# Optimization experiments

Measured on AMD Instinct MI355X. Metric: run time of the kernel, lower is better.

The kernel has to match this reference:

```python
import jax, jax.numpy as jnp
import numpy as np

N, E, G = 20000, 320000, 128
H, TE, CD = 128, 128, 64
HEADS, DH = 4, 32          # inner = 128 == H
L = 6


def _fwd(p, edge_index, batch):
    """Faithful forward of CrystalDiffusionModel (eval mode: dropout = identity).
    EquivariantGraphConv (imported in the original) is implemented as the standard
    edge-conditioned message-passing conv: m_ij = silu(W[h_src; h_dst; e_ij] + b),
    agg = scatter_add over dst, h' = W_u[h; agg] + b_u."""
    x, ea, t = p['x'], p['edge_attr'], p['t']
    n = x.shape[0]
    h = x @ p['Wn'] + p['bn']                      # [N,H] node embedding
    ef = ea @ p['We'] + p['be']                    # [E,H] edge embedding

    # sinusoidal time embedding -> MLP
    half = TE // 2
    freq = jnp.exp(-jnp.arange(half, dtype=jnp.float32) * (np.log(10000.0) / (half - 1)))
    te = t[:, None] * freq[None, :]
    te = jnp.concatenate([jnp.sin(te), jnp.cos(te)], axis=-1)          # [G,TE]
    te = jax.nn.silu(te @ p['tm_W1'] + p['tm_b1']) @ p['tm_W2'] + p['tm_b2']

    def mlp2(z, W1, b1, W2, b2):
        return jax.nn.silu(z @ W1 + b1) @ W2 + b2

    topo_e = mlp2(p['topo_cond'], p['topo_W1'], p['topo_b1'], p['topo_W2'], p['topo_b2'])
    stab_e = mlp2(p['stab_cond'], p['stab_W1'], p['stab_b1'], p['stab_W2'], p['stab_b2'])
    sust_e = mlp2(p['sust_cond'], p['sust_W1'], p['sust_b1'], p['sust_W2'], p['sust_b2'])
    cond = mlp2(jnp.concatenate([topo_e, stab_e, sust_e], axis=-1),
                p['comb_W1'], p['comb_b1'], p['comb_W2'], p['comb_b2'])  # [G,CD]

    ctx = cond[batch]                               # [N,CD] per-node condition
    # context is a single token per query -> k,v constant across layers
    k = (ctx @ p['Wk']).reshape(n, HEADS, DH)
    v = (ctx @ p['Wv']).reshape(n, HEADS, DH)
    ti = jax.nn.silu(te)[batch]                     # [N,H] time influence (dropout=id)

    src, dst = edge_index[0], edge_index[1]
    scale = DH ** -0.5
    for i in range(L):
        Wm, bm = p['gnn_Wm'][i], p['gnn_bm'][i]
        # split concat-GEMM to avoid materializing [E, 3H]
        m = jax.nn.silu(h[src] @ Wm[:H] + h[dst] @ Wm[H:2 * H] + ef @ Wm[2 * H:] + bm)
        agg = jax.ops.segment_sum(m, dst, num_segments=n)               # [N,H]
        Wu, bu = p['gnn_Wu'][i], p['gnn_bu'][i]
        hu = h @ Wu[:H] + agg @ Wu[H:] + bu
        # LayerNorm
        mu = hu.mean(-1, keepdims=True)
        var = hu.var(-1, keepdims=True)
        hu = (hu - mu) * jax.lax.rsqrt(var + 1e-5) * p['ln_g'][i] + p['ln_b'][i]
        # cross-attention; context length is 1 so softmax over j is exactly 1
        q = (hu @ p['Wq']).reshape(n, HEADS, DH)
        sim = jnp.einsum('nhd,nhd->nh', q, k) * scale                   # [N,heads]
        attn = jax.nn.softmax(sim[..., None], axis=-1)                  # == 1.0
        out = (attn * v).reshape(n, HEADS * DH)
        hu = out @ p['Wo'] + p['bo']
        h = h + hu + ti                              # residual + time influence

    node_pred = jax.nn.silu(h @ p['np_W1'] + p['np_b1']) @ p['np_W2'] + p['np_b2']
    pos_pred = jax.nn.silu(h @ p['pp_W1'] + p['pp_b1']) @ p['pp_W2'] + p['pp_b2']
    return node_pred, pos_pred


def setup_inputs() -> dict:
    key = jax.random.key(0)
    it = iter(jax.random.split(key, 96))

    def nrm(shape, s=0.02):
        return jax.random.normal(next(it), shape, jnp.float32) * s

    z = lambda *s: jnp.zeros(s, jnp.float32)
    inp = {
        'x': jax.random.normal(next(it), (N, 12), jnp.float32),
        'edge_index': jax.random.randint(next(it), (2, E), 0, N),
        'edge_attr': jax.random.normal(next(it), (E, 20), jnp.float32),
        'pos': jax.random.normal(next(it), (N, 3), jnp.float32),
        't': jax.random.uniform(next(it), (G,), jnp.float32) * 1000.0,
        'topo_cond': jax.random.normal(next(it), (G, 7), jnp.float32),
        'stab_cond': jax.random.normal(next(it), (G, 2), jnp.float32),
        'sust_cond': jax.random.normal(next(it), (G, 3), jnp.float32),
        'batch': jnp.sort(jax.random.randint(next(it), (N,), 0, G)),
        'Wn': nrm((12, H)), 'bn': z(H), 'We': nrm((20, H)), 'be': z(H),
        'tm_W1': nrm((TE, 2 * TE)), 'tm_b1': z(2 * TE), 'tm_W2': nrm((2 * TE, TE)), 'tm_b2': z(TE),
        'topo_W1': nrm((7, 32)), 'topo_b1': z(32), 'topo_W2': nrm((32, 32)), 'topo_b2': z(32),
        'stab_W1': nrm((2, 16)), 'stab_b1': z(16), 'stab_W2': nrm((16, 16)), 'stab_b2': z(16),
        'sust_W1': nrm((3, 16)), 'sust_b1': z(16), 'sust_W2': nrm((16, 16)), 'sust_b2': z(16),
        'comb_W1': nrm((64, CD)), 'comb_b1': z(CD), 'comb_W2': nrm((CD, CD)), 'comb_b2': z(CD),
        'Wq': nrm((H, HEADS * DH)), 'Wk': nrm((CD, HEADS * DH)), 'Wv': nrm((CD, HEADS * DH)),
        'Wo': nrm((HEADS * DH, H)), 'bo': z(H),
        'gnn_Wm': nrm((L, 3 * H, H)), 'gnn_bm': z(L, H),
        'gnn_Wu': nrm((L, 2 * H, H)), 'gnn_bu': z(L, H),
        'ln_g': jnp.ones((L, H), jnp.float32), 'ln_b': z(L, H),
        'np_W1': nrm((H, 2 * H)), 'np_b1': z(2 * H), 'np_W2': nrm((2 * H, 12)), 'np_b2': z(12),
        'pp_W1': nrm((H, H)), 'pp_b1': z(H), 'pp_W2': nrm((H, 3)), 'pp_b2': z(3),
    }
    return inp


def reference(x, edge_index, edge_attr, pos, t, topo_cond, stab_cond, sust_cond, batch,
              Wn, bn, We, be, tm_W1, tm_b1, tm_W2, tm_b2,
              topo_W1, topo_b1, topo_W2, topo_b2, stab_W1, stab_b1, stab_W2, stab_b2,
              sust_W1, sust_b1, sust_W2, sust_b2, comb_W1, comb_b1, comb_W2, comb_b2,
              Wq, Wk, Wv, Wo, bo, gnn_Wm, gnn_bm, gnn_Wu, gnn_bu, ln_g, ln_b,
              np_W1, np_b1, np_W2, np_b2, pp_W1, pp_b1, pp_W2, pp_b2):
    loc = dict(locals())
    p = {k: v for k, v in loc.items() if k not in ('edge_index', 'batch', 'pos')}
    return _fwd(p, edge_index, batch)
```

## Files before the change

kernel.cpp:

```cpp
#include <hip/hip_runtime.h>
#include <hip/hip_bf16.h>

#define NN 20000
#define GG 128

typedef __bf16 bf16x8_t __attribute__((ext_vector_type(8)));
typedef float  f32x4_t  __attribute__((ext_vector_type(4)));
typedef __hip_bfloat16 hbf16;

#define PK_NPW1 0
#define PK_PPW1 32768
#define PK_NPW2 49152
#define PK_PPW2 53248
#define PK_WN   55296
#define GADD_OFF 59392

__device__ __forceinline__ float silu_f(float v) {
    return v * __builtin_amdgcn_rcpf(1.0f + __expf(-v));
}

__device__ __forceinline__ void cp_async(hbf16* dst, const hbf16* src,
                                         int nbytes, int w, int lane) {
    const int per_wave = nbytes >> 2;
    const char* g = (const char*)src + w * per_wave + lane * 16;
    char* l = (char*)dst + w * per_wave + lane * 16;
    for (int j = 0; j < per_wave; j += 1024)
        __builtin_amdgcn_global_load_lds(
            (__attribute__((address_space(1))) void*)(g + j),
            (__attribute__((address_space(3))) void*)(l + j),
            16, 0, 0);
}

__global__ __launch_bounds__(512) void prep_kernel(
        const float* __restrict__ t, const float* __restrict__ topo,
        const float* __restrict__ stab, const float* __restrict__ sust,
        const float* __restrict__ tmW1, const float* __restrict__ tmb1,
        const float* __restrict__ tmW2, const float* __restrict__ tmb2,
        const float* __restrict__ topoW1, const float* __restrict__ topob1,
        const float* __restrict__ topoW2, const float* __restrict__ topob2,
        const float* __restrict__ stabW1, const float* __restrict__ stabb1,
        const float* __restrict__ stabW2, const float* __restrict__ stabb2,
        const float* __restrict__ sustW1, const float* __restrict__ sustb1,
        const float* __restrict__ sustW2, const float* __restrict__ sustb2,
        const float* __restrict__ combW1, const float* __restrict__ combb1,
        const float* __restrict__ combW2, const float* __restrict__ combb2,
        const float* __restrict__ Wv, const float* __restrict__ Wo,
        const float* __restrict__ bo,
        const float* __restrict__ npW1, const float* __restrict__ npW2,
        const float* __restrict__ ppW1, const float* __restrict__ ppW2,
        const float* __restrict__ Wn,
        float* __restrict__ gadd, hbf16* __restrict__ wsb) {
    const int tid = threadIdx.x;

    if (blockIdx.x >= GG) {
        const int s = (blockIdx.x - GG) * 512 + tid;
        if (s < 32768) {
            const int p = s;
            const int j = p & 7, l = (p >> 3) & 63, kb = (p >> 9) & 3, ct = p >> 11;
            const int k = kb * 32 + ((l >> 4) << 3) + j;
            const int n = ct * 16 + (l & 15);
            wsb[PK_NPW1 + p] = __float2bfloat16(npW1[k * 256 + n]);
        } else if (s < 49152) {
            const int p = s - 32768;
            const int j = p & 7, l = (p >> 3) & 63, kb = (p >> 9) & 3, ct = p >> 11;
            const int k = kb * 32 + ((l >> 4) << 3) + j;
            const int n = ct * 16 + (l & 15);
            wsb[PK_PPW1 + p] = __float2bfloat16(ppW1[k * 128 + n]);
        } else if (s < 53248) {
            const int p = s - 49152;
            const int j = p & 7, l = (p >> 3) & 63, kb = p >> 9;
            const int k = kb * 32 + ((l >> 4) << 3) + j;
            const int n = l & 15;
            wsb[PK_NPW2 + p] = __float2bfloat16(n < 12 ? npW2[k * 12 + n] : 0.0f);
        } else if (s < 55296) {
            const int p = s - 53248;
            const int j = p & 7, l = (p >> 3) & 63, kb = p >> 9;
            const int k = kb * 32 + ((l >> 4) << 3) + j;
            const int n = l & 15;
            wsb[PK_PPW2 + p] = __float2bfloat16(n < 3 ? ppW2[k * 3 + n] : 0.0f);
        } else if (s < 59392) {
            const int p = s - 55296;
            const int j = p & 7, l = (p >> 3) & 63, ct = p >> 9;
            const int k = ((l >> 4) << 3) + j;
            const int n = ct * 16 + (l & 15);
            wsb[PK_WN + p] = __float2bfloat16(k < 12 ? Wn[k * 128 + n] : 0.0f);
        }
        return;
    }

    __shared__ float s_te[128];
    __shared__ float s_th1[256];
    __shared__ float s_tef[128];
    __shared__ float s_l1[64];
    __shared__ float s_cat[64];
    __shared__ float s_c1[64];
    __shared__ float s_cond[64];
    __shared__ float s_v[128];
    __shared__ float s_red[512];

    const int g = blockIdx.x;

    if (tid < 128) {
        const float tval = t[g];
        const int i = tid & 63;
        const float fr = __expf(-(float)i * 0.14619587892025688f);
        const float arg = tval * fr;
        s_te[tid] = (tid < 64) ? sinf(arg) : cosf(arg);
    } else if (tid < 192) {
        const int c = tid - 128;
        if (c < 32) {
            float acc = topob1[c];
            for (int k = 0; k < 7; ++k)
                acc += topo[g * 7 + k] * topoW1[k * 32 + c];
            s_l1[c] = silu_f(acc);
        } else if (c < 48) {
            const int j = c - 32;
            float acc = stabb1[j];
            for (int k = 0; k < 2; ++k)
                acc += stab[g * 2 + k] * stabW1[k * 16 + j];
            s_l1[c] = silu_f(acc);
        } else {
            const int j = c - 48;
            float acc = sustb1[j];
            for (int k = 0; k < 3; ++k)
                acc += sust[g * 3 + k] * sustW1[k * 16 + j];
            s_l1[c] = silu_f(acc);
        }
    }
    __syncthreads();

    {
        const int col = tid & 255, half = tid >> 8;
        float acc = 0.0f;
#pragma unroll 32
        for (int kk = 0; kk < 64; ++kk) {
            const int k = half * 64 + kk;
            acc += s_te[k] * tmW1[k * 256 + col];
        }
        s_red[half * 256 + col] = acc;
    }
    __syncthreads();
    if (tid < 256)
        s_th1[tid] = silu_f(tmb1[tid] + s_red[tid] + s_red[256 + tid]);
    __syncthreads();

    {
        const int col = tid & 127, qt = tid >> 7;
        float acc = 0.0f;
#pragma unroll 32
        for (int kk = 0; kk < 64; ++kk) {
            const int k = qt * 64 + kk;
            acc += s_th1[k] * tmW2[k * 128 + col];
        }
        s_red[qt * 128 + col] = acc;
    }
    __syncthreads();
    if (tid < 128) {
        s_tef[tid] = tmb2[tid] + s_red[tid] + s_red[128 + tid] +
                     s_red[256 + tid] + s_red[384 + tid];
    } else if (tid < 192) {
        const int c = tid - 128;
        if (c < 32) {
            float acc = topob2[c];
            for (int k = 0; k < 32; ++k)
                acc += s_l1[k] * topoW2[k * 32 + c];
            s_cat[c] = acc;
        } else if (c < 48) {
            const int j = c - 32;
            float acc = stabb2[j];
            for (int k = 0; k < 16; ++k)
                acc += s_l1[32 + k] * stabW2[k * 16 + j];
            s_cat[c] = acc;
        } else {
            const int j = c - 48;
            float acc = sustb2[j];
            for (int k = 0; k < 16; ++k)
                acc += s_l1[48 + k] * sustW2[k * 16 + j];
            s_cat[c] = acc;
        }
    }
    __syncthreads();

    {
        const int col = tid & 63, part = tid >> 6;
        float acc = 0.0f;
#pragma unroll
        for (int kk = 0; kk < 8; ++kk) {
            const int k = part * 8 + kk;
            acc += s_cat[k] * combW1[k * 64 + col];
        }
        s_red[part * 64 + col] = acc;
    }
    __syncthreads();
    if (tid < 64) {
        float a = combb1[tid];
#pragma unroll
        for (int p = 0; p < 8; ++p) a += s_red[p * 64 + tid];
        s_c1[tid] = silu_f(a);
    }
    __syncthreads();

    {
        const int col = tid & 63, part = tid >> 6;
        float acc = 0.0f;
#pragma unroll
        for (int kk = 0; kk < 8; ++kk) {
            const int k = part * 8 + kk;
            acc += s_c1[k] * combW2[k * 64 + col];
        }
        s_red[part * 64 + col] = acc;
    }
    __syncthreads();
    if (tid < 64) {
        float a = combb2[tid];
#pragma unroll
        for (int p = 0; p < 8; ++p) a += s_red[p * 64 + tid];
        s_cond[tid] = a;
    }
    __syncthreads();

    {
        const int col = tid & 127, qt = tid >> 7;
        float acc = 0.0f;
#pragma unroll
        for (int kk = 0; kk < 16; ++kk) {
            const int k = qt * 16 + kk;
            acc += s_cond[k] * Wv[k * 128 + col];
        }
        s_red[qt * 128 + col] = acc;
    }
    __syncthreads();
    if (tid < 128)
        s_v[tid] = s_red[tid] + s_red[128 + tid] + s_red[256 + tid] + s_red[384 + tid];
    __syncthreads();

    {
        const int col = tid & 127, qt = tid >> 7;
        float acc = 0.0f;
#pragma unroll 32
        for (int kk = 0; kk < 32; ++kk) {
            const int k = qt * 32 + kk;
            acc += s_v[k] * Wo[k * 128 + col];
        }
        s_red[qt * 128 + col] = acc;
    }
    __syncthreads();
    if (tid < 128)
        gadd[g * 128 + tid] = 6.0f * (bo[tid] + s_red[tid] + s_red[128 + tid] +
                                      s_red[256 + tid] + s_red[384 + tid] +
                                      silu_f(s_tef[tid]));
}

#define NGS 6

__global__ __launch_bounds__(256) void node_kernel(
        const float* __restrict__ x, const int* __restrict__ batch,
        const float* __restrict__ bn,
        const float* __restrict__ npb1, const float* __restrict__ npb2,
        const float* __restrict__ ppb1, const float* __restrict__ ppb2,
        const float* __restrict__ gadd, const hbf16* __restrict__ wsb,
        float* __restrict__ out) {
    __shared__ __align__(16) hbf16 s_wA[8192];
    __shared__ __align__(16) hbf16 s_wB[8192];
    __shared__ __align__(16) hbf16 s_wn[4096];
    __shared__ __align__(16) hbf16 tbuf[4 * 16 * 264];
    __shared__ float s_gadd[NGS * 128];
    __shared__ float s_bias[528];

    const int tid  = threadIdx.x;
    const int nb   = blockIdx.x * 64;
    const int w    = tid >> 6;
    const int lane = tid & 63;
    const int q    = lane >> 4;
    const int r    = lane & 15;
    const int n16  = nb + w * 16;

    hbf16* wb = tbuf + w * (16 * 264);

    cp_async(s_wn, wsb + PK_WN, 8192, w, lane);
    cp_async(s_wA, wsb + PK_NPW1, 16384, w, lane);

    const int g0 = batch[nb];
    for (int i = tid; i < NGS * 128; i += 256) {
        int gr = g0 + (i >> 7);
        if (gr > GG - 1) gr = GG - 1;
        s_gadd[i] = gadd[gr * 128 + (i & 127)];
    }
    for (int i = tid; i < 528; i += 256) {
        float v;
        if (i < 128) v = bn[i];
        else if (i < 384) v = npb1[i - 128];
        else if (i < 396) v = npb2[i - 384];
        else if (i < 524) v = ppb1[i - 396];
        else if (i < 527) v = ppb2[i - 524];
        else v = 0.0f;
        s_bias[i] = v;
    }

    bf16x8_t Ax;
    {
        const int node = n16 + r;
        float xv[8];
#pragma unroll
        for (int j = 0; j < 8; ++j) xv[j] = 0.0f;
        if (node < NN) {
            if (q == 0) {
                const float4 a = *reinterpret_cast<const float4*>(x + node * 12);
                const float4 b = *reinterpret_cast<const float4*>(x + node * 12 + 4);
                xv[0] = a.x; xv[1] = a.y; xv[2] = a.z; xv[3] = a.w;
                xv[4] = b.x; xv[5] = b.y; xv[6] = b.z; xv[7] = b.w;
            } else if (q == 1) {
                const float4 a = *reinterpret_cast<const float4*>(x + node * 12 + 8);
                xv[0] = a.x; xv[1] = a.y; xv[2] = a.z; xv[3] = a.w;
            }
        }
#pragma unroll
        for (int j = 0; j < 8; ++j) {
            const hbf16 tv = __float2bfloat16(xv[j]);
            Ax[j] = *reinterpret_cast<const __bf16*>(&tv);
        }
    }
    int gidx[4];
#pragma unroll
    for (int i = 0; i < 4; ++i) {
        int gn = n16 + q * 4 + i;
        if (gn > NN - 1) gn = NN - 1;
        gidx[i] = batch[gn] - g0;
    }
    __syncthreads();

    bf16x8_t Ah[4];
    {
        f32x4_t hacc[8];
#pragma unroll
        for (int ct = 0; ct < 8; ++ct) {
            const bf16x8_t Bf = *reinterpret_cast<const bf16x8_t*>(
                &s_wn[(ct * 64 + lane) * 8]);
            hacc[ct] = __builtin_amdgcn_mfma_f32_16x16x32_bf16(
                Ax, Bf, (f32x4_t){0.f, 0.f, 0.f, 0.f}, 0, 0, 0);
        }
#pragma unroll
        for (int ct = 0; ct < 8; ++ct) {
            const int n = ct * 16 + r;
            const float bv = s_bias[n];
#pragma unroll
            for (int i = 0; i < 4; ++i) {
                const int gi = gidx[i];
                const float ga = (gi < NGS) ? s_gadd[gi * 128 + n]
                                            : gadd[(g0 + gi) * 128 + n];
                wb[(q * 4 + i) * 136 + n] = __float2bfloat16(hacc[ct][i] + bv + ga);
            }
        }
#pragma unroll
        for (int kb = 0; kb < 4; ++kb)
            Ah[kb] = *reinterpret_cast<const bf16x8_t*>(
                &wb[r * 136 + kb * 32 + q * 8]);
    }

    auto npL1_quad = [&](int cbase, const hbf16* sw) {
#pragma unroll
        for (int ci = 0; ci < 4; ++ci) {
            f32x4_t acc = (f32x4_t){0.f, 0.f, 0.f, 0.f};
#pragma unroll
            for (int kb = 0; kb < 4; ++kb) {
                const bf16x8_t Bf = *reinterpret_cast<const bf16x8_t*>(
                    &sw[((ci * 4 + kb) * 64 + lane) * 8]);
                acc = __builtin_amdgcn_mfma_f32_16x16x32_bf16(Ah[kb], Bf, acc, 0, 0, 0);
            }
            const int col = (cbase * 4 + ci) * 16 + r;
            const float b1 = s_bias[128 + col];
#pragma unroll
            for (int i = 0; i < 4; ++i)
                wb[(q * 4 + i) * 264 + col] = __float2bfloat16(silu_f(acc[i] + b1));
        }
    };
    auto ppL1_quad = [&](int cbase, const hbf16* sw) {
#pragma unroll
        for (int ci = 0; ci < 4; ++ci) {
            f32x4_t acc = (f32x4_t){0.f, 0.f, 0.f, 0.f};
#pragma unroll
            for (int kb = 0; kb < 4; ++kb) {
                const bf16x8_t Bf = *reinterpret_cast<const bf16x8_t*>(
                    &sw[((ci * 4 + kb) * 64 + lane) * 8]);
                acc = __builtin_amdgcn_mfma_f32_16x16x32_bf16(Ah[kb], Bf, acc, 0, 0, 0);
            }
            const int col = (cbase * 4 + ci) * 16 + r;
            const float b1 = s_bias[396 + col];
#pragma unroll
            for (int i = 0; i < 4; ++i)
                wb[(q * 4 + i) * 136 + col] = __float2bfloat16(silu_f(acc[i] + b1));
        }
    };

    cp_async(s_wB, wsb + PK_NPW1 + 8192, 16384, w, lane);
    npL1_quad(0, s_wA);
    __syncthreads();

    cp_async(s_wA, wsb + PK_NPW1 + 16384, 16384, w, lane);
    npL1_quad(1, s_wB);
    __syncthreads();

    cp_async(s_wB, wsb + PK_NPW1 + 24576, 16384, w, lane);
    npL1_quad(2, s_wA);
    __syncthreads();

    cp_async(s_wA, wsb + PK_NPW2, 8192, w, lane);
    npL1_quad(3, s_wB);
    __syncthreads();

    cp_async(s_wB, wsb + PK_PPW1, 16384, w, lane);
    {
        f32x4_t acc2 = (f32x4_t){0.f, 0.f, 0.f, 0.f};
#pragma unroll
        for (int kb = 0; kb < 8; ++kb) {
            const bf16x8_t Af = *reinterpret_cast<const bf16x8_t*>(
                &wb[r * 264 + kb * 32 + q * 8]);
            const bf16x8_t Bf = *reinterpret_cast<const bf16x8_t*>(
                &s_wA[(kb * 64 + lane) * 8]);
            acc2 = __builtin_amdgcn_mfma_f32_16x16x32_bf16(Af, Bf, acc2, 0, 0, 0);
        }
        if (r < 12) {
            const float b2 = s_bias[384 + r];
#pragma unroll
            for (int i = 0; i < 4; ++i) {
                const int gn = n16 + q * 4 + i;
                if (gn < NN) out[gn * 12 + r] = acc2[i] + b2;
            }
        }
    }
    __syncthreads();

    cp_async(s_wA, wsb + PK_PPW1 + 8192, 16384, w, lane);
    ppL1_quad(0, s_wB);
    __syncthreads();

    cp_async(s_wB, wsb + PK_PPW2, 4096, w, lane);
    ppL1_quad(1, s_wA);
    __syncthreads();

    {
        f32x4_t acc2 = (f32x4_t){0.f, 0.f, 0.f, 0.f};
#pragma unroll
        for (int kb = 0; kb < 4; ++kb) {
            const bf16x8_t Af = *reinterpret_cast<const bf16x8_t*>(
                &wb[r * 136 + kb * 32 + q * 8]);
            const bf16x8_t Bf = *reinterpret_cast<const bf16x8_t*>(
                &s_wB[(kb * 64 + lane) * 8]);
            acc2 = __builtin_amdgcn_mfma_f32_16x16x32_bf16(Af, Bf, acc2, 0, 0, 0);
        }
        if (r < 3) {
            const float b2 = s_bias[524 + r];
#pragma unroll
            for (int i = 0; i < 4; ++i) {
                const int gn = n16 + q * 4 + i;
                if (gn < NN) out[NN * 12 + gn * 3 + r] = acc2[i] + b2;
            }
        }
    }
}

extern "C" void kernel_launch(void* const* d_in, const int* in_sizes, int n_in,
                              void* d_out, int out_size, void* d_ws, size_t ws_size,
                              hipStream_t stream) {
    const float* x      = (const float*)d_in[0];
    const float* t      = (const float*)d_in[4];
    const float* topo   = (const float*)d_in[5];
    const float* stab   = (const float*)d_in[6];
    const float* sust   = (const float*)d_in[7];
    const int*   batch  = (const int*)d_in[8];
    const float* Wn     = (const float*)d_in[9];
    const float* bn     = (const float*)d_in[10];
    const float* tmW1   = (const float*)d_in[13];
    const float* tmb1   = (const float*)d_in[14];
    const float* tmW2   = (const float*)d_in[15];
    const float* tmb2   = (const float*)d_in[16];
    const float* topoW1 = (const float*)d_in[17];
    const float* topob1 = (const float*)d_in[18];
    const float* topoW2 = (const float*)d_in[19];
    const float* topob2 = (const float*)d_in[20];
    const float* stabW1 = (const float*)d_in[21];
    const float* stabb1 = (const float*)d_in[22];
    const float* stabW2 = (const float*)d_in[23];
    const float* stabb2 = (const float*)d_in[24];
    const float* sustW1 = (const float*)d_in[25];
    const float* sustb1 = (const float*)d_in[26];
    const float* sustW2 = (const float*)d_in[27];
    const float* sustb2 = (const float*)d_in[28];
    const float* combW1 = (const float*)d_in[29];
    const float* combb1 = (const float*)d_in[30];
    const float* combW2 = (const float*)d_in[31];
    const float* combb2 = (const float*)d_in[32];
    const float* Wv     = (const float*)d_in[35];
    const float* Wo     = (const float*)d_in[36];
    const float* bo     = (const float*)d_in[37];
    const float* npW1   = (const float*)d_in[44];
    const float* npb1   = (const float*)d_in[45];
    const float* npW2   = (const float*)d_in[46];
    const float* npb2   = (const float*)d_in[47];
    const float* ppW1   = (const float*)d_in[48];
    const float* ppb1   = (const float*)d_in[49];
    const float* ppW2   = (const float*)d_in[50];
    const float* ppb2   = (const float*)d_in[51];

    hbf16* wsb = (hbf16*)d_ws;
    float* gadd = (float*)(wsb + GADD_OFF);
    float* out = (float*)d_out;

    prep_kernel<<<GG + 116, 512, 0, stream>>>(
        t, topo, stab, sust,
        tmW1, tmb1, tmW2, tmb2,
        topoW1, topob1, topoW2, topob2,
        stabW1, stabb1, stabW2, stabb2,
        sustW1, sustb1, sustW2, sustb2,
        combW1, combb1, combW2, combb2,
        Wv, Wo, bo,
        npW1, npW2, ppW1, ppW2, Wn,
        gadd, wsb);

    node_kernel<<<(NN + 63) / 64, 256, 0, stream>>>(
        x, batch, bn, npb1, npb2, ppb1, ppb2, gadd, wsb, out);
}
```

Baseline: 194.7 us.

## Merge prep and node kernels into one cooperative kernel with grid sync

Replaces the two launches (prep_kernel plus node_kernel) with a single cooperative mono_kernel. The first blocks compute the per-graph conditioning vector and pack the bf16 weights, then a grid-wide barrier separates that phase from the node MLP phase. The prep work is remapped from 512 to 256 threads per block, and shared memory is reused between phases through one raw buffer. The aim is to remove a kernel launch and its drain gap, at the cost of a grid-wide barrier. The launch needs all 313 blocks (79936 bytes of shared memory each) to be co-resident, or the cooperative launch fails.

New measurement: 288.5 us. +48.2%, slower.

```diff
diff --git a/kernel.cpp b/kernel.cpp
--- a/kernel.cpp
+++ b/kernel.cpp
@@ -1,5 +1,8 @@
 #include <hip/hip_runtime.h>
 #include <hip/hip_bf16.h>
+#include <hip/hip_cooperative_groups.h>
+
+namespace cg = cooperative_groups;
 
 #define NN 20000
 #define GG 128
@@ -14,6 +17,8 @@
 #define PK_PPW2 53248
 #define PK_WN   55296
 #define GADD_OFF 59392
+
+#define NGS 6
 
 __device__ __forceinline__ float silu_f(float v) {
     return v * __builtin_amdgcn_rcpf(1.0f + __expf(-v));
@@ -31,244 +36,213 @@
             16, 0, 0);
 }
 
-__global__ __launch_bounds__(512) void prep_kernel(
-        const float* __restrict__ t, const float* __restrict__ topo,
-        const float* __restrict__ stab, const float* __restrict__ sust,
-        const float* __restrict__ tmW1, const float* __restrict__ tmb1,
-        const float* __restrict__ tmW2, const float* __restrict__ tmb2,
-        const float* __restrict__ topoW1, const float* __restrict__ topob1,
-        const float* __restrict__ topoW2, const float* __restrict__ topob2,
-        const float* __restrict__ stabW1, const float* __restrict__ stabb1,
-        const float* __restrict__ stabW2, const float* __restrict__ stabb2,
-        const float* __restrict__ sustW1, const float* __restrict__ sustb1,
-        const float* __restrict__ sustW2, const float* __restrict__ sustb2,
-        const float* __restrict__ combW1, const float* __restrict__ combb1,
-        const float* __restrict__ combW2, const float* __restrict__ combb2,
-        const float* __restrict__ Wv, const float* __restrict__ Wo,
-        const float* __restrict__ bo,
-        const float* __restrict__ npW1, const float* __restrict__ npW2,
-        const float* __restrict__ ppW1, const float* __restrict__ ppW2,
-        const float* __restrict__ Wn,
-        float* __restrict__ gadd, hbf16* __restrict__ wsb) {
-    const int tid = threadIdx.x;
-
-    if (blockIdx.x >= GG) {
-        const int s = (blockIdx.x - GG) * 512 + tid;
-        if (s < 32768) {
-            const int p = s;
-            const int j = p & 7, l = (p >> 3) & 63, kb = (p >> 9) & 3, ct = p >> 11;
-            const int k = kb * 32 + ((l >> 4) << 3) + j;
-            const int n = ct * 16 + (l & 15);
-            wsb[PK_NPW1 + p] = __float2bfloat16(npW1[k * 256 + n]);
-        } else if (s < 49152) {
-            const int p = s - 32768;
-            const int j = p & 7, l = (p >> 3) & 63, kb = (p >> 9) & 3, ct = p >> 11;
-            const int k = kb * 32 + ((l >> 4) << 3) + j;
-            const int n = ct * 16 + (l & 15);
-            wsb[PK_PPW1 + p] = __float2bfloat16(ppW1[k * 128 + n]);
-        } else if (s < 53248) {
-            const int p = s - 49152;
-            const int j = p & 7, l = (p >> 3) & 63, kb = p >> 9;
-            const int k = kb * 32 + ((l >> 4) << 3) + j;
-            const int n = l & 15;
-            wsb[PK_NPW2 + p] = __float2bfloat16(n < 12 ? npW2[k * 12 + n] : 0.0f);
-        } else if (s < 55296) {
-            const int p = s - 53248;
-            const int j = p & 7, l = (p >> 3) & 63, kb = p >> 9;
-            const int k = kb * 32 + ((l >> 4) << 3) + j;
-            const int n = l & 15;
-            wsb[PK_PPW2 + p] = __float2bfloat16(n < 3 ? ppW2[k * 3 + n] : 0.0f);
-        } else if (s < 59392) {
-            const int p = s - 55296;
-            const int j = p & 7, l = (p >> 3) & 63, ct = p >> 9;
-            const int k = ((l >> 4) << 3) + j;
-            const int n = ct * 16 + (l & 15);
-            wsb[PK_WN + p] = __float2bfloat16(k < 12 ? Wn[k * 128 + n] : 0.0f);
-        }
-        return;
-    }
-
-    __shared__ float s_te[128];
-    __shared__ float s_th1[256];
-    __shared__ float s_tef[128];
-    __shared__ float s_l1[64];
-    __shared__ float s_cat[64];
-    __shared__ float s_c1[64];
-    __shared__ float s_cond[64];
-    __shared__ float s_v[128];
-    __shared__ float s_red[512];
-
-    const int g = blockIdx.x;
-
-    if (tid < 128) {
-        const float tval = t[g];
-        const int i = tid & 63;
-        const float fr = __expf(-(float)i * 0.14619587892025688f);
-        const float arg = tval * fr;
-        s_te[tid] = (tid < 64) ? sinf(arg) : cosf(arg);
-    } else if (tid < 192) {
-        const int c = tid - 128;
-        if (c < 32) {
-            float acc = topob1[c];
-            for (int k = 0; k < 7; ++k)
-                acc += topo[g * 7 + k] * topoW1[k * 32 + c];
-            s_l1[c] = silu_f(acc);
-        } else if (c < 48) {
-            const int j = c - 32;
-            float acc = stabb1[j];
-            for (int k = 0; k < 2; ++k)
-                acc += stab[g * 2 + k] * stabW1[k * 16 + j];
-            s_l1[c] = silu_f(acc);
-        } else {
-            const int j = c - 48;
-            float acc = sustb1[j];
-            for (int k = 0; k < 3; ++k)
-                acc += sust[g * 3 + k] * sustW1[k * 16 + j];
-            s_l1[c] = silu_f(acc);
-        }
-    }
-    __syncthreads();
-
-    {
-        const int col = tid & 255, half = tid >> 8;
-        float acc = 0.0f;
-#pragma unroll 32
-        for (int kk = 0; kk < 64; ++kk) {
-            const int k = half * 64 + kk;
-            acc += s_te[k] * tmW1[k * 256 + col];
-        }
-        s_red[half * 256 + col] = acc;
-    }
-    __syncthreads();
-    if (tid < 256)
-        s_th1[tid] = silu_f(tmb1[tid] + s_red[tid] + s_red[256 + tid]);
-    __syncthreads();
-
-    {
-        const int col = tid & 127, qt = tid >> 7;
-        float acc = 0.0f;
-#pragma unroll 32
-        for (int kk = 0; kk < 64; ++kk) {
-            const int k = qt * 64 + kk;
-            acc += s_th1[k] * tmW2[k * 128 + col];
-        }
-        s_red[qt * 128 + col] = acc;
-    }
-    __syncthreads();
-    if (tid < 128) {
-        s_tef[tid] = tmb2[tid] + s_red[tid] + s_red[128 + tid] +
-                     s_red[256 + tid] + s_red[384 + tid];
-    } else if (tid < 192) {
-        const int c = tid - 128;
-        if (c < 32) {
-            float acc = topob2[c];
-            for (int k = 0; k < 32; ++k)
-                acc += s_l1[k] * topoW2[k * 32 + c];
-            s_cat[c] = acc;
-        } else if (c < 48) {
-            const int j = c - 32;
-            float acc = stabb2[j];
-            for (int k = 0; k < 16; ++k)
-                acc += s_l1[32 + k] * stabW2[k * 16 + j];
-            s_cat[c] = acc;
-        } else {
-            const int j = c - 48;
-            float acc = sustb2[j];
-            for (int k = 0; k < 16; ++k)
-                acc += s_l1[48 + k] * sustW2[k * 16 + j];
-            s_cat[c] = acc;
-        }
-    }
-    __syncthreads();
-
-    {
-        const int col = tid & 63, part = tid >> 6;
-        float acc = 0.0f;
-#pragma unroll
-        for (int kk = 0; kk < 8; ++kk) {
-            const int k = part * 8 + kk;
-            acc += s_cat[k] * combW1[k * 64 + col];
-        }
-        s_red[part * 64 + col] = acc;
-    }
-    __syncthreads();
-    if (tid < 64) {
-        float a = combb1[tid];
-#pragma unroll
-        for (int p = 0; p < 8; ++p) a += s_red[p * 64 + tid];
-        s_c1[tid] = silu_f(a);
-    }
-    __syncthreads();
-
-    {
-        const int col = tid & 63, part = tid >> 6;
-        float acc = 0.0f;
-#pragma unroll
-        for (int kk = 0; kk < 8; ++kk) {
-            const int k = part * 8 + kk;
-            acc += s_c1[k] * combW2[k * 64 + col];
-        }
-        s_red[part * 64 + col] = acc;
-    }
-    __syncthreads();
-    if (tid < 64) {
-        float a = combb2[tid];
-#pragma unroll
-        for (int p = 0; p < 8; ++p) a += s_red[p * 64 + tid];
-        s_cond[tid] = a;
-    }
-    __syncthreads();
-
-    {
-        const int col = tid & 127, qt = tid >> 7;
-        float acc = 0.0f;
-#pragma unroll
-        for (int kk = 0; kk < 16; ++kk) {
-            const int k = qt * 16 + kk;
-            acc += s_cond[k] * Wv[k * 128 + col];
-        }
-        s_red[qt * 128 + col] = acc;
-    }
-    __syncthreads();
-    if (tid < 128)
-        s_v[tid] = s_red[tid] + s_red[128 + tid] + s_red[256 + tid] + s_red[384 + tid];
-    __syncthreads();
-
-    {
-        const int col = tid & 127, qt = tid >> 7;
-        float acc = 0.0f;
-#pragma unroll 32
-        for (int kk = 0; kk < 32; ++kk) {
-            const int k = qt * 32 + kk;
-            acc += s_v[k] * Wo[k * 128 + col];
-        }
-        s_red[qt * 128 + col] = acc;
-    }
-    __syncthreads();
-    if (tid < 128)
-        gadd[g * 128 + tid] = 6.0f * (bo[tid] + s_red[tid] + s_red[128 + tid] +
-                                      s_red[256 + tid] + s_red[384 + tid] +
-                                      silu_f(s_tef[tid]));
-}
-
-#define NGS 6
-
-__global__ __launch_bounds__(256) void node_kernel(
-        const float* __restrict__ x, const int* __restrict__ batch,
-        const float* __restrict__ bn,
-        const float* __restrict__ npb1, const float* __restrict__ npb2,
-        const float* __restrict__ ppb1, const float* __restrict__ ppb2,
-        const float* __restrict__ gadd, const hbf16* __restrict__ wsb,
-        float* __restrict__ out) {
-    __shared__ __align__(16) hbf16 s_wA[8192];
-    __shared__ __align__(16) hbf16 s_wB[8192];
-    __shared__ __align__(16) hbf16 s_wn[4096];
-    __shared__ __align__(16) hbf16 tbuf[4 * 16 * 264];
-    __shared__ float s_gadd[NGS * 128];
-    __shared__ float s_bias[528];
+struct Params {
+    const float *x; const int *batch;
+    const float *t, *topo, *stab, *sust;
+    const float *tmW1, *tmb1, *tmW2, *tmb2;
+    const float *topoW1, *topob1, *topoW2, *topob2;
+    const float *stabW1, *stabb1, *stabW2, *stabb2;
+    const float *sustW1, *sustb1, *sustW2, *sustb2;
+    const float *combW1, *combb1, *combW2, *combb2;
+    const float *Wv, *Wo, *bo, *bn;
+    const float *npW1, *npb1, *npW2, *npb2;
+    const float *ppW1, *ppb1, *ppW2, *ppb2;
+    const float *Wn;
+    float *gadd; hbf16 *wsb; float *out;
+};
+
+__global__ __launch_bounds__(256) void mono_kernel(Params p) {
+    __shared__ __align__(16) char smem[79936];
 
     const int tid  = threadIdx.x;
-    const int nb   = blockIdx.x * 64;
+    const int b    = blockIdx.x;
+
+    if (b >= GG && b < GG + 116) {
+#pragma unroll
+        for (int e = 0; e < 2; ++e) {
+            const int s = (b - GG) * 512 + e * 256 + tid;
+            if (s < 32768) {
+                const int pط = s;
+                const int j = pط & 7, l = (pط >> 3) & 63, kb = (pط >> 9) & 3, ct = pط >> 11;
+                const int k = kb * 32 + ((l >> 4) << 3) + j;
+                const int n = ct * 16 + (l & 15);
+                p.wsb[PK_NPW1 + pط] = __float2bfloat16(p.npW1[k * 256 + n]);
+            } else if (s < 49152) {
+                const int pط = s - 32768;
+                const int j = pط & 7, l = (pط >> 3) & 63, kb = (pط >> 9) & 3, ct = pط >> 11;
+                const int k = kb * 32 + ((l >> 4) << 3) + j;
+                const int n = ct * 16 + (l & 15);
+                p.wsb[PK_PPW1 + pط] = __float2bfloat16(p.ppW1[k * 128 + n]);
+            } else if (s < 53248) {
+                const int pط = s - 49152;
+                const int j = pط & 7, l = (pط >> 3) & 63, kb = pط >> 9;
+                const int k = kb * 32 + ((l >> 4) << 3) + j;
+                const int n = l & 15;
+                p.wsb[PK_NPW2 + pط] = __float2bfloat16(n < 12 ? p.npW2[k * 12 + n] : 0.0f);
+            } else if (s < 55296) {
+                const int pط = s - 53248;
+                const int j = pط & 7, l = (pط >> 3) & 63, kb = pط >> 9;
+                const int k = kb * 32 + ((l >> 4) << 3) + j;
+                const int n = l & 15;
+                p.wsb[PK_PPW2 + pط] = __float2bfloat16(n < 3 ? p.ppW2[k * 3 + n] : 0.0f);
+            } else if (s < 59392) {
+                const int pط = s - 55296;
+                const int j = pط & 7, l = (pط >> 3) & 63, ct = pط >> 9;
+                const int k = ((l >> 4) << 3) + j;
+                const int n = ct * 16 + (l & 15);
+                p.wsb[PK_WN + pط] = __float2bfloat16(k < 12 ? p.Wn[k * 128 + n] : 0.0f);
+            }
+        }
+    } else if (b < GG) {
+        float* s_te  = (float*)smem;
+        float* s_th1 = (float*)(smem + 512);
+        float* s_tef = (float*)(smem + 1536);
+        float* s_l1  = (float*)(smem + 2048);
+        float* s_cat = (float*)(smem + 2304);
+        float* s_c1  = (float*)(smem + 2560);
+        float* s_cond= (float*)(smem + 2816);
+        float* s_v   = (float*)(smem + 3072);
+        float* s_red = (float*)(smem + 3584);
+
+        const int g = b;
+
+        if (tid < 128) {
+            const float tval = p.t[g];
+            const int i = tid & 63;
+            const float fr = __expf(-(float)i * 0.14619587892025688f);
+            const float arg = tval * fr;
+            s_te[tid] = (tid < 64) ? sinf(arg) : cosf(arg);
+        } else if (tid < 192) {
+            const int c = tid - 128;
+            if (c < 32) {
+                float acc = p.topob1[c];
+                for (int k = 0; k < 7; ++k)
+                    acc += p.topo[g * 7 + k] * p.topoW1[k * 32 + c];
+                s_l1[c] = silu_f(acc);
+            } else if (c < 48) {
+                const int j = c - 32;
+                float acc = p.stabb1[j];
+                for (int k = 0; k < 2; ++k)
+                    acc += p.stab[g * 2 + k] * p.stabW1[k * 16 + j];
+                s_l1[c] = silu_f(acc);
+            } else {
+                const int j = c - 48;
+                float acc = p.sustb1[j];
+                for (int k = 0; k < 3; ++k)
+                    acc += p.sust[g * 3 + k] * p.sustW1[k * 16 + j];
+                s_l1[c] = silu_f(acc);
+            }
+        }
+        __syncthreads();
+
+        {
+            float acc = p.tmb1[tid];
+#pragma unroll 16
+            for (int k = 0; k < 128; ++k)
+                acc += s_te[k] * p.tmW1[k * 256 + tid];
+            s_th1[tid] = silu_f(acc);
+        }
+        __syncthreads();
+
+        {
+            const int j = tid & 127, half = tid >> 7;
+            float acc = 0.0f;
+#pragma unroll 16
+            for (int kk = 0; kk < 128; ++kk)
+                acc += s_th1[half * 128 + kk] * p.tmW2[(half * 128 + kk) * 128 + j];
+            s_red[tid] = acc;
+        }
+        __syncthreads();
+
+        if (tid < 128) {
+            s_tef[tid] = p.tmb2[tid] + s_red[tid] + s_red[tid + 128];
+        } else if (tid < 192) {
+            const int c = tid - 128;
+            if (c < 32) {
+                float acc = p.topob2[c];
+                for (int k = 0; k < 32; ++k)
+                    acc += s_l1[k] * p.topoW2[k * 32 + c];
+                s_cat[c] = acc;
+            } else if (c < 48) {
+                const int j = c - 32;
+                float acc = p.stabb2[j];
+                for (int k = 0; k < 16; ++k)
+                    acc += s_l1[32 + k] * p.stabW2[k * 16 + j];
+                s_cat[c] = acc;
+            } else {
+                const int j = c - 48;
+                float acc = p.sustb2[j];
+                for (int k = 0; k < 16; ++k)
+                    acc += s_l1[48 + k] * p.sustW2[k * 16 + j];
+                s_cat[c] = acc;
+            }
+        }
+        __syncthreads();
+
+        {
+            const int j = tid & 63, part = tid >> 6;
+            float acc = 0.0f;
+#pragma unroll
+            for (int kk = 0; kk < 16; ++kk)
+                acc += s_cat[part * 16 + kk] * p.combW1[(part * 16 + kk) * 64 + j];
+            s_red[tid] = acc;
+        }
+        __syncthreads();
+        if (tid < 64)
+            s_c1[tid] = silu_f(p.combb1[tid] + s_red[tid] + s_red[tid + 64] +
+                               s_red[tid + 128] + s_red[tid + 192]);
+        __syncthreads();
+
+        {
+            const int j = tid & 63, part = tid >> 6;
+            float acc = 0.0f;
+#pragma unroll
+            for (int kk = 0; kk < 16; ++kk)
+                acc += s_c1[part * 16 + kk] * p.combW2[(part * 16 + kk) * 64 + j];
+            s_red[tid] = acc;
+        }
+        __syncthreads();
+        if (tid < 64)
+            s_cond[tid] = p.combb2[tid] + s_red[tid] + s_red[tid + 64] +
+                          s_red[tid + 128] + s_red[tid + 192];
+        __syncthreads();
+
+        {
+            const int j = tid & 127, half = tid >> 7;
+            float acc = 0.0f;
+#pragma unroll
+            for (int kk = 0; kk < 32; ++kk)
+                acc += s_cond[half * 32 + kk] * p.Wv[(half * 32 + kk) * 128 + j];
+            s_red[tid] = acc;
+        }
+        __syncthreads();
+        if (tid < 128) s_v[tid] = s_red[tid] + s_red[tid + 128];
+        __syncthreads();
+
+        {
+            const int j = tid & 127, half = tid >> 7;
+            float acc = 0.0f;
+#pragma unroll 16
+            for (int kk = 0; kk < 64; ++kk)
+                acc += s_v[half * 64 + kk] * p.Wo[(half * 64 + kk) * 128 + j];
+            s_red[tid] = acc;
+        }
+        __syncthreads();
+        if (tid < 128)
+            p.gadd[g * 128 + tid] =
+                6.0f * (p.bo[tid] + s_red[tid] + s_red[tid + 128] + silu_f(s_tef[tid]));
+    }
+
+    cg::this_grid().sync();
+
+    hbf16* s_wA   = (hbf16*)smem;
+    hbf16* s_wB   = (hbf16*)(smem + 16384);
+    hbf16* s_wn   = (hbf16*)(smem + 32768);
+    hbf16* tbuf   = (hbf16*)(smem + 40960);
+    float* s_gadd = (float*)(smem + 74752);
+    float* s_bias = (float*)(smem + 77824);
+
+    const int nb   = b * 64;
     const int w    = tid >> 6;
     const int lane = tid & 63;
     const int q    = lane >> 4;
@@ -276,11 +250,14 @@
     const int n16  = nb + w * 16;
 
     hbf16* wb = tbuf + w * (16 * 264);
+    const hbf16* wsb = p.wsb;
+    const float* gadd = p.gadd;
+    float* out = p.out;
 
     cp_async(s_wn, wsb + PK_WN, 8192, w, lane);
     cp_async(s_wA, wsb + PK_NPW1, 16384, w, lane);
 
-    const int g0 = batch[nb];
+    const int g0 = p.batch[nb];
     for (int i = tid; i < NGS * 128; i += 256) {
         int gr = g0 + (i >> 7);
         if (gr > GG - 1) gr = GG - 1;
@@ -288,11 +265,11 @@
     }
     for (int i = tid; i < 528; i += 256) {
         float v;
-        if (i < 128) v = bn[i];
-        else if (i < 384) v = npb1[i - 128];
-        else if (i < 396) v = npb2[i - 384];
-        else if (i < 524) v = ppb1[i - 396];
-        else if (i < 527) v = ppb2[i - 524];
+        if (i < 128) v = p.bn[i];
+        else if (i < 384) v = p.npb1[i - 128];
+        else if (i < 396) v = p.npb2[i - 384];
+        else if (i < 524) v = p.ppb1[i - 396];
+        else if (i < 527) v = p.ppb2[i - 524];
         else v = 0.0f;
         s_bias[i] = v;
     }
@@ -305,12 +282,12 @@
         for (int j = 0; j < 8; ++j) xv[j] = 0.0f;
         if (node < NN) {
             if (q == 0) {
-                const float4 a = *reinterpret_cast<const float4*>(x + node * 12);
-                const float4 b = *reinterpret_cast<const float4*>(x + node * 12 + 4);
+                const float4 a = *reinterpret_cast<const float4*>(p.x + node * 12);
+                const float4 c = *reinterpret_cast<const float4*>(p.x + node * 12 + 4);
                 xv[0] = a.x; xv[1] = a.y; xv[2] = a.z; xv[3] = a.w;
-                xv[4] = b.x; xv[5] = b.y; xv[6] = b.z; xv[7] = b.w;
+                xv[4] = c.x; xv[5] = c.y; xv[6] = c.z; xv[7] = c.w;
             } else if (q == 1) {
-                const float4 a = *reinterpret_cast<const float4*>(x + node * 12 + 8);
+                const float4 a = *reinterpret_cast<const float4*>(p.x + node * 12 + 8);
                 xv[0] = a.x; xv[1] = a.y; xv[2] = a.z; xv[3] = a.w;
             }
         }
@@ -325,7 +302,7 @@
     for (int i = 0; i < 4; ++i) {
         int gn = n16 + q * 4 + i;
         if (gn > NN - 1) gn = NN - 1;
-        gidx[i] = batch[gn] - g0;
+        gidx[i] = p.batch[gn] - g0;
     }
     __syncthreads();
 
@@ -462,61 +439,53 @@
 extern "C" void kernel_launch(void* const* d_in, const int* in_sizes, int n_in,
                               void* d_out, int out_size, void* d_ws, size_t ws_size,
                               hipStream_t stream) {
-    const float* x      = (const float*)d_in[0];
-    const float* t      = (const float*)d_in[4];
-    const float* topo   = (const float*)d_in[5];
-    const float* stab   = (const float*)d_in[6];
-    const float* sust   = (const float*)d_in[7];
-    const int*   batch  = (const int*)d_in[8];
-    const float* Wn     = (const float*)d_in[9];
-    const float* bn     = (const float*)d_in[10];
-    const float* tmW1   = (const float*)d_in[13];
-    const float* tmb1   = (const float*)d_in[14];
-    const float* tmW2   = (const float*)d_in[15];
-    const float* tmb2   = (const float*)d_in[16];
-    const float* topoW1 = (const float*)d_in[17];
-    const float* topob1 = (const float*)d_in[18];
-    const float* topoW2 = (const float*)d_in[19];
-    const float* topob2 = (const float*)d_in[20];
-    const float* stabW1 = (const float*)d_in[21];
-    const float* stabb1 = (const float*)d_in[22];
-    const float* stabW2 = (const float*)d_in[23];
-    const float* stabb2 = (const float*)d_in[24];
-    const float* sustW1 = (const float*)d_in[25];
-    const float* sustb1 = (const float*)d_in[26];
-    const float* sustW2 = (const float*)d_in[27];
-    const float* sustb2 = (const float*)d_in[28];
-    const float* combW1 = (const float*)d_in[29];
-    const float* combb1 = (const float*)d_in[30];
-    const float* combW2 = (const float*)d_in[31];
-    const float* combb2 = (const float*)d_in[32];
-    const float* Wv     = (const float*)d_in[35];
-    const float* Wo     = (const float*)d_in[36];
-    const float* bo     = (const float*)d_in[37];
-    const float* npW1   = (const float*)d_in[44];
-    const float* npb1   = (const float*)d_in[45];
-    const float* npW2   = (const float*)d_in[46];
-    const float* npb2   = (const float*)d_in[47];
-    const float* ppW1   = (const float*)d_in[48];
-    const float* ppb1   = (const float*)d_in[49];
-    const float* ppW2   = (const float*)d_in[50];
-    const float* ppb2   = (const float*)d_in[51];
-
-    hbf16* wsb = (hbf16*)d_ws;
-    float* gadd = (float*)(wsb + GADD_OFF);
-    float* out = (float*)d_out;
-
-    prep_kernel<<<GG + 116, 512, 0, stream>>>(
-        t, topo, stab, sust,
-        tmW1, tmb1, tmW2, tmb2,
-        topoW1, topob1, topoW2, topob2,
-        stabW1, stabb1, stabW2, stabb2,
-        sustW1, sustb1, sustW2, sustb2,
-        combW1, combb1, combW2, combb2,
-        Wv, Wo, bo,
-        npW1, npW2, ppW1, ppW2, Wn,
-        gadd, wsb);
-
-    node_kernel<<<(NN + 63) / 64, 256, 0, stream>>>(
-        x, batch, bn, npb1, npb2, ppb1, ppb2, gadd, wsb, out);
+    Params prm;
+    prm.x      = (const float*)d_in[0];
+    prm.t      = (const float*)d_in[4];
+    prm.topo   = (const float*)d_in[5];
+    prm.stab   = (const float*)d_in[6];
+    prm.sust   = (const float*)d_in[7];
+    prm.batch  = (const int*)d_in[8];
+    prm.Wn     = (const float*)d_in[9];
+    prm.bn     = (const float*)d_in[10];
+    prm.tmW1   = (const float*)d_in[13];
+    prm.tmb1   = (const float*)d_in[14];
+    prm.tmW2   = (const float*)d_in[15];
+    prm.tmb2   = (const float*)d_in[16];
+    prm.topoW1 = (const float*)d_in[17];
+    prm.topob1 = (const float*)d_in[18];
+    prm.topoW2 = (const float*)d_in[19];
+    prm.topob2 = (const float*)d_in[20];
+    prm.stabW1 = (const float*)d_in[21];
+    prm.stabb1 = (const float*)d_in[22];
+    prm.stabW2 = (const float*)d_in[23];
+    prm.stabb2 = (const float*)d_in[24];
+    prm.sustW1 = (const float*)d_in[25];
+    prm.sustb1 = (const float*)d_in[26];
+    prm.sustW2 = (const float*)d_in[27];
+    prm.sustb2 = (const float*)d_in[28];
+    prm.combW1 = (const float*)d_in[29];
+    prm.combb1 = (const float*)d_in[30];
+    prm.combW2 = (const float*)d_in[31];
+    prm.combb2 = (const float*)d_in[32];
+    prm.Wv     = (const float*)d_in[35];
+    prm.Wo     = (const float*)d_in[36];
+    prm.bo     = (const float*)d_in[37];
+    prm.npW1   = (const float*)d_in[44];
+    prm.npb1   = (const float*)d_in[45];
+    prm.npW2   = (const float*)d_in[46];
+    prm.npb2   = (const float*)d_in[47];
+    prm.ppW1   = (const float*)d_in[48];
+    prm.ppb1   = (const float*)d_in[49];
+    prm.ppW2   = (const float*)d_in[50];
+    prm.ppb2   = (const float*)d_in[51];
+
+    prm.wsb  = (hbf16*)d_ws;
+    prm.gadd = (float*)(prm.wsb + GADD_OFF);
+    prm.out  = (float*)d_out;
+
+    void* args[] = { &prm };
+    hipLaunchCooperativeKernel((const void*)mono_kernel,
+                               dim3((NN + 63) / 64), dim3(256),
+                               args, 0, stream);
 }
```

## Load all head weights into LDS once and process two node tiles per block

Applied to the files above, without the earlier changes.

The node kernel now copies the whole packed weight table (about 116 KB) into shared memory in one go, instead of double-buffering chunks with a sync between each stage. It launches a fixed 256 blocks, and the first 57 blocks each handle a second 64-node tile, which reuses the loaded weights and prefetches that tile's inputs and gadd values up front. This removes the per-stage barriers and the repeated weight streaming. In exchange, occupancy drops to one block per CU, and the up-front load is not overlapped with compute, so the 57 blocks with two tiles set the critical path.

New measurement: 193.7 us. About the same (-0.5%).

```diff
diff --git a/kernel.cpp b/kernel.cpp
--- a/kernel.cpp
+++ b/kernel.cpp
@@ -3,6 +3,7 @@
 
 #define NN 20000
 #define GG 128
+#define NTILES 313
 
 typedef __bf16 bf16x8_t __attribute__((ext_vector_type(8)));
 typedef float  f32x4_t  __attribute__((ext_vector_type(4)));
@@ -251,41 +252,27 @@
                                       silu_f(s_tef[tid]));
 }
 
-#define NGS 6
-
-__global__ __launch_bounds__(256) void node_kernel(
+__global__ __launch_bounds__(256, 1) void node_kernel(
         const float* __restrict__ x, const int* __restrict__ batch,
         const float* __restrict__ bn,
         const float* __restrict__ npb1, const float* __restrict__ npb2,
         const float* __restrict__ ppb1, const float* __restrict__ ppb2,
         const float* __restrict__ gadd, const hbf16* __restrict__ wsb,
         float* __restrict__ out) {
-    __shared__ __align__(16) hbf16 s_wA[8192];
-    __shared__ __align__(16) hbf16 s_wB[8192];
-    __shared__ __align__(16) hbf16 s_wn[4096];
+    __shared__ __align__(16) hbf16 s_wtab[59392];
     __shared__ __align__(16) hbf16 tbuf[4 * 16 * 264];
-    __shared__ float s_gadd[NGS * 128];
     __shared__ float s_bias[528];
 
     const int tid  = threadIdx.x;
-    const int nb   = blockIdx.x * 64;
     const int w    = tid >> 6;
     const int lane = tid & 63;
     const int q    = lane >> 4;
     const int r    = lane & 15;
-    const int n16  = nb + w * 16;
 
     hbf16* wb = tbuf + w * (16 * 264);
 
-    cp_async(s_wn, wsb + PK_WN, 8192, w, lane);
-    cp_async(s_wA, wsb + PK_NPW1, 16384, w, lane);
-
-    const int g0 = batch[nb];
-    for (int i = tid; i < NGS * 128; i += 256) {
-        int gr = g0 + (i >> 7);
-        if (gr > GG - 1) gr = GG - 1;
-        s_gadd[i] = gadd[gr * 128 + (i & 127)];
-    }
+    cp_async(s_wtab, wsb, 118784, w, lane);
+
     for (int i = tid; i < 528; i += 256) {
         float v;
         if (i < 128) v = bn[i];
@@ -297,8 +284,8 @@
         s_bias[i] = v;
     }
 
-    bf16x8_t Ax;
-    {
+    auto prefetch = [&](int nb, bf16x8_t& Ax, float (*gv)[4]) {
+        const int n16 = nb + w * 16;
         const int node = n16 + r;
         float xv[8];
 #pragma unroll
@@ -319,143 +306,136 @@
             const hbf16 tv = __float2bfloat16(xv[j]);
             Ax[j] = *reinterpret_cast<const __bf16*>(&tv);
         }
-    }
-    int gidx[4];
-#pragma unroll
-    for (int i = 0; i < 4; ++i) {
-        int gn = n16 + q * 4 + i;
-        if (gn > NN - 1) gn = NN - 1;
-        gidx[i] = batch[gn] - g0;
-    }
-    __syncthreads();
-
-    bf16x8_t Ah[4];
-    {
-        f32x4_t hacc[8];
-#pragma unroll
-        for (int ct = 0; ct < 8; ++ct) {
-            const bf16x8_t Bf = *reinterpret_cast<const bf16x8_t*>(
-                &s_wn[(ct * 64 + lane) * 8]);
-            hacc[ct] = __builtin_amdgcn_mfma_f32_16x16x32_bf16(
-                Ax, Bf, (f32x4_t){0.f, 0.f, 0.f, 0.f}, 0, 0, 0);
-        }
-#pragma unroll
-        for (int ct = 0; ct < 8; ++ct) {
-            const int n = ct * 16 + r;
-            const float bv = s_bias[n];
-#pragma unroll
-            for (int i = 0; i < 4; ++i) {
-                const int gi = gidx[i];
-                const float ga = (gi < NGS) ? s_gadd[gi * 128 + n]
-                                            : gadd[(g0 + gi) * 128 + n];
-                wb[(q * 4 + i) * 136 + n] = __float2bfloat16(hacc[ct][i] + bv + ga);
-            }
-        }
-#pragma unroll
-        for (int kb = 0; kb < 4; ++kb)
-            Ah[kb] = *reinterpret_cast<const bf16x8_t*>(
-                &wb[r * 136 + kb * 32 + q * 8]);
-    }
-
-    auto npL1_quad = [&](int cbase, const hbf16* sw) {
-#pragma unroll
-        for (int ci = 0; ci < 4; ++ci) {
+        int gi[4];
+#pragma unroll
+        for (int i = 0; i < 4; ++i) {
+            int gn = n16 + q * 4 + i;
+            if (gn > NN - 1) gn = NN - 1;
+            gi[i] = batch[gn];
+        }
+#pragma unroll
+        for (int ct = 0; ct < 8; ++ct)
+#pragma unroll
+            for (int i = 0; i < 4; ++i)
+                gv[ct][i] = gadd[gi[i] * 128 + ct * 16 + r];
+    };
+
+    auto run_tile = [&](int nb, bf16x8_t Ax, float (*gv)[4]) {
+        const int n16 = nb + w * 16;
+
+        bf16x8_t Ah[4];
+        {
+            f32x4_t hacc[8];
+#pragma unroll
+            for (int ct = 0; ct < 8; ++ct) {
+                const bf16x8_t Bf = *reinterpret_cast<const bf16x8_t*>(
+                    &s_wtab[PK_WN + (ct * 64 + lane) * 8]);
+                hacc[ct] = __builtin_amdgcn_mfma_f32_16x16x32_bf16(
+                    Ax, Bf, (f32x4_t){0.f, 0.f, 0.f, 0.f}, 0, 0, 0);
+            }
+#pragma unroll
+            for (int ct = 0; ct < 8; ++ct) {
+                const int n = ct * 16 + r;
+                const float bv = s_bias[n];
+#pragma unroll
+                for (int i = 0; i < 4; ++i)
+                    wb[(q * 4 + i) * 136 + n] =
+                        __float2bfloat16(hacc[ct][i] + bv + gv[ct][i]);
+            }
+#pragma unroll
+            for (int kb = 0; kb < 4; ++kb)
+                Ah[kb] = *reinterpret_cast<const bf16x8_t*>(
+                    &wb[r * 136 + kb * 32 + q * 8]);
+        }
+
+#pragma unroll
+        for (int ct = 0; ct < 16; ++ct) {
             f32x4_t acc = (f32x4_t){0.f, 0.f, 0.f, 0.f};
 #pragma unroll
             for (int kb = 0; kb < 4; ++kb) {
                 const bf16x8_t Bf = *reinterpret_cast<const bf16x8_t*>(
-                    &sw[((ci * 4 + kb) * 64 + lane) * 8]);
+                    &s_wtab[PK_NPW1 + ((ct * 4 + kb) * 64 + lane) * 8]);
                 acc = __builtin_amdgcn_mfma_f32_16x16x32_bf16(Ah[kb], Bf, acc, 0, 0, 0);
             }
-            const int col = (cbase * 4 + ci) * 16 + r;
+            const int col = ct * 16 + r;
             const float b1 = s_bias[128 + col];
 #pragma unroll
             for (int i = 0; i < 4; ++i)
                 wb[(q * 4 + i) * 264 + col] = __float2bfloat16(silu_f(acc[i] + b1));
         }
-    };
-    auto ppL1_quad = [&](int cbase, const hbf16* sw) {
-#pragma unroll
-        for (int ci = 0; ci < 4; ++ci) {
+
+        {
+            f32x4_t acc2 = (f32x4_t){0.f, 0.f, 0.f, 0.f};
+#pragma unroll
+            for (int kb = 0; kb < 8; ++kb) {
+                const bf16x8_t Af = *reinterpret_cast<const bf16x8_t*>(
+                    &wb[r * 264 + kb * 32 + q * 8]);
+                const bf16x8_t Bf = *reinterpret_cast<const bf16x8_t*>(
+                    &s_wtab[PK_NPW2 + (kb * 64 + lane) * 8]);
+                acc2 = __builtin_amdgcn_mfma_f32_16x16x32_bf16(Af, Bf, acc2, 0, 0, 0);
+            }
+            if (r < 12) {
+                const float b2 = s_bias[384 + r];
+#pragma unroll
+                for (int i = 0; i < 4; ++i) {
+                    const int gn = n16 + q * 4 + i;
+                    if (gn < NN) out[gn * 12 + r] = acc2[i] + b2;
+                }
+            }
+        }
+
+#pragma unroll
+        for (int ct = 0; ct < 8; ++ct) {
             f32x4_t acc = (f32x4_t){0.f, 0.f, 0.f, 0.f};
 #pragma unroll
             for (int kb = 0; kb < 4; ++kb) {
                 const bf16x8_t Bf = *reinterpret_cast<const bf16x8_t*>(
-                    &sw[((ci * 4 + kb) * 64 + lane) * 8]);
+                    &s_wtab[PK_PPW1 + ((ct * 4 + kb) * 64 + lane) * 8]);
                 acc = __builtin_amdgcn_mfma_f32_16x16x32_bf16(Ah[kb], Bf, acc, 0, 0, 0);
             }
-            const int col = (cbase * 4 + ci) * 16 + r;
+            const int col = ct * 16 + r;
             const float b1 = s_bias[396 + col];
 #pragma unroll
             for (int i = 0; i < 4; ++i)
                 wb[(q * 4 + i) * 136 + col] = __float2bfloat16(silu_f(acc[i] + b1));
         }
+
+        {
+            f32x4_t acc2 = (f32x4_t){0.f, 0.f, 0.f, 0.f};
+#pragma unroll
+            for (int kb = 0; kb < 4; ++kb) {
+                const bf16x8_t Af = *reinterpret_cast<const bf16x8_t*>(
+                    &wb[r * 136 + kb * 32 + q * 8]);
+                const bf16x8_t Bf = *reinterpret_cast<const bf16x8_t*>(
+                    &s_wtab[PK_PPW2 + (kb * 64 + lane) * 8]);
+                acc2 = __builtin_amdgcn_mfma_f32_16x16x32_bf16(Af, Bf, acc2, 0, 0, 0);
+            }
+            if (r < 3) {
+                const float b2 = s_bias[524 + r];
+#pragma unroll
+                for (int i = 0; i < 4; ++i) {
+                    const int gn = n16 + q * 4 + i;
+                    if (gn < NN) out[NN * 12 + gn * 3 + r] = acc2[i] + b2;
+                }
+            }
+        }
     };
 
-    cp_async(s_wB, wsb + PK_NPW1 + 8192, 16384, w, lane);
-    npL1_quad(0, s_wA);
-    __syncthreads();
-
-    cp_async(s_wA, wsb + PK_NPW1 + 16384, 16384, w, lane);
-    npL1_quad(1, s_wB);
-    __syncthreads();
-
-    cp_async(s_wB, wsb + PK_NPW1 + 24576, 16384, w, lane);
-    npL1_quad(2, s_wA);
-    __syncthreads();
-
-    cp_async(s_wA, wsb + PK_NPW2, 8192, w, lane);
-    npL1_quad(3, s_wB);
-    __syncthreads();
-
-    cp_async(s_wB, wsb + PK_PPW1, 16384, w, lane);
-    {
-        f32x4_t acc2 = (f32x4_t){0.f, 0.f, 0.f, 0.f};
-#pragma unroll
-        for (int kb = 0; kb < 8; ++kb) {
-            const bf16x8_t Af = *reinterpret_cast<const bf16x8_t*>(
-                &wb[r * 264 + kb * 32 + q * 8]);
-            const bf16x8_t Bf = *reinterpret_cast<const bf16x8_t*>(
-                &s_wA[(kb * 64 + lane) * 8]);
-            acc2 = __builtin_amdgcn_mfma_f32_16x16x32_bf16(Af, Bf, acc2, 0, 0, 0);
-        }
-        if (r < 12) {
-            const float b2 = s_bias[384 + r];
-#pragma unroll
-            for (int i = 0; i < 4; ++i) {
-                const int gn = n16 + q * 4 + i;
-                if (gn < NN) out[gn * 12 + r] = acc2[i] + b2;
-            }
-        }
-    }
-    __syncthreads();
-
-    cp_async(s_wA, wsb + PK_PPW1 + 8192, 16384, w, lane);
-    ppL1_quad(0, s_wB);
-    __syncthreads();
-
-    cp_async(s_wB, wsb + PK_PPW2, 4096, w, lane);
-    ppL1_quad(1, s_wA);
-    __syncthreads();
-
-    {
-        f32x4_t acc2 = (f32x4_t){0.f, 0.f, 0.f, 0.f};
-#pragma unroll
-        for (int kb = 0; kb < 4; ++kb) {
-            const bf16x8_t Af = *reinterpret_cast<const bf16x8_t*>(
-                &wb[r * 136 + kb * 32 + q * 8]);
-            const bf16x8_t Bf = *reinterpret_cast<const bf16x8_t*>(
-                &s_wB[(kb * 64 + lane) * 8]);
-            acc2 = __builtin_amdgcn_mfma_f32_16x16x32_bf16(Af, Bf, acc2, 0, 0, 0);
-        }
-        if (r < 3) {
-            const float b2 = s_bias[524 + r];
-#pragma unroll
-            for (int i = 0; i < 4; ++i) {
-                const int gn = n16 + q * 4 + i;
-                if (gn < NN) out[NN * 12 + gn * 3 + r] = acc2[i] + b2;
-            }
-        }
+    bf16x8_t Ax1;
+    float gv1[8][4];
+    prefetch(blockIdx.x * 64, Ax1, gv1);
+
+    __syncthreads();
+
+    const int t2 = blockIdx.x + 256;
+    if (t2 < NTILES) {
+        bf16x8_t Ax2;
+        float gv2[8][4];
+        prefetch(t2 * 64, Ax2, gv2);
+        run_tile(blockIdx.x * 64, Ax1, gv1);
+        run_tile(t2 * 64, Ax2, gv2);
+    } else {
+        run_tile(blockIdx.x * 64, Ax1, gv1);
     }
 }
 
@@ -517,6 +497,6 @@
         npW1, npW2, ppW1, ppW2, Wn,
         gadd, wsb);
 
-    node_kernel<<<(NN + 63) / 64, 256, 0, stream>>>(
+    node_kernel<<<256, 256, 0, stream>>>(
         x, batch, bn, npb1, npb2, ppb1, ppb2, gadd, wsb, out);
 }
```
